# Performance work log

Measured on AMD Instinct MI355X. Metric: run time of the kernel, lower is better.

Reference implementation:

```python
import jax, jax.numpy as jnp
import numpy as np
import math

N = 20000      # nodes
E = 150000     # edges
IN = 256       # in_dim
HID = 256      # n_hid / out_dim
T = 4          # num_types
R = 8          # num_relations
H = 8          # n_heads
DK = HID // H  # d_k = 32
L = 2          # n_layers
MAXLEN = 240   # RTE max_len


def _rte_table():
    # fixed sinusoid table from RelTemporalEncoding (requires_grad=False in torch)
    pos = np.arange(MAXLEN, dtype=np.float64)[:, None]
    div = np.exp(np.arange(0, HID, 2, dtype=np.float64) * -(math.log(10000.0) / HID))
    emb = np.zeros((MAXLEN, HID), dtype=np.float64)
    emb[:, 0::2] = np.sin(pos * div) / math.sqrt(HID)
    emb[:, 1::2] = np.cos(pos * div) / math.sqrt(HID)
    return jnp.asarray(emb, dtype=jnp.float32)


def setup_inputs() -> dict:
    key = jax.random.key(0)
    ks = jax.random.split(key, 20)
    node_feature = jax.random.normal(ks[0], (N, IN), jnp.float32)
    node_type = jax.random.randint(ks[1], (N,), 0, T)
    edge_index = jax.random.randint(ks[2], (2, E), 0, N)
    edge_type = jax.random.randint(ks[3], (E,), 0, R)
    edge_time = jax.random.randint(ks[4], (E,), 0, MAXLEN)

    s_in = 1.0 / math.sqrt(IN)
    s_h = 1.0 / math.sqrt(HID)
    s_g = math.sqrt(2.0 / (DK + DK))  # glorot for relation mats

    adapt_W = jax.random.normal(ks[5], (T, IN, HID), jnp.float32) * s_in
    adapt_b = jnp.zeros((T, HID), jnp.float32)
    k_W = jax.random.normal(ks[6], (L, T, HID, HID), jnp.float32) * s_h
    k_b = jnp.zeros((L, T, HID), jnp.float32)
    q_W = jax.random.normal(ks[7], (L, T, HID, HID), jnp.float32) * s_h
    q_b = jnp.zeros((L, T, HID), jnp.float32)
    v_W = jax.random.normal(ks[8], (L, T, HID, HID), jnp.float32) * s_h
    v_b = jnp.zeros((L, T, HID), jnp.float32)
    a_W = jax.random.normal(ks[9], (L, T, HID, HID), jnp.float32) * s_h
    a_b = jnp.zeros((L, T, HID), jnp.float32)
    rel_pri = jnp.ones((L, R, H), jnp.float32)
    rel_att = jax.random.normal(ks[10], (L, R, H, DK, DK), jnp.float32) * s_g
    rel_msg = jax.random.normal(ks[11], (L, R, H, DK, DK), jnp.float32) * s_g
    skip = jnp.ones((L, T), jnp.float32)
    rte_W = jax.random.normal(ks[12], (L, HID, HID), jnp.float32) * s_h
    rte_b = jnp.zeros((L, HID), jnp.float32)
    rte_emb = _rte_table()

    return dict(node_feature=node_feature, node_type=node_type, edge_time=edge_time,
                edge_index=edge_index, edge_type=edge_type,
                adapt_W=adapt_W, adapt_b=adapt_b, k_W=k_W, k_b=k_b, q_W=q_W, q_b=q_b,
                v_W=v_W, v_b=v_b, a_W=a_W, a_b=a_b, rel_pri=rel_pri, rel_att=rel_att,
                rel_msg=rel_msg, skip=skip, rte_W=rte_W, rte_b=rte_b, rte_emb=rte_emb)


def _typed_linear(x, W, b, types):
    # x: [M, din]; W: [T, din, dout]; per-row type-selected linear (T dense GEMMs + select)
    out = jnp.zeros((x.shape[0], W.shape[-1]), x.dtype)
    for t in range(T):
        out = jnp.where((types == t)[:, None], x @ W[t] + b[t], out)
    return out


def _hgt_forward(node_feature, node_type, edge_time, edge_index, edge_type,
                 adapt_W, adapt_b, k_W, k_b, q_W, q_b, v_W, v_b, a_W, a_b,
                 rel_pri, rel_att, rel_msg, skip, rte_W, rte_b, rte_emb):
    # adapt: per-type tanh(Linear) (dropout is identity at p=0)
    x = jnp.tanh(_typed_linear(node_feature, adapt_W, adapt_b, node_type))
    src, tgt = edge_index[0], edge_index[1]   # j (source), i (target)
    st, tt = node_type[src], node_type[tgt]
    sqrt_dk = math.sqrt(DK)
    att = None
    rte = rte_emb[edge_time]                  # [E, HID]
    for l in range(L):
        x_j = x[src] + (rte @ rte_W[l] + rte_b[l])   # RTE added to source repr
        x_i = x[tgt]
        q = _typed_linear(x_i, q_W[l], q_b[l], tt).reshape(E, H, DK)
        k = _typed_linear(x_j, k_W[l], k_b[l], st).reshape(E, H, DK)
        v = _typed_linear(x_j, v_W[l], v_b[l], st).reshape(E, H, DK)
        att_e = jnp.zeros((E, H), x.dtype)
        msg = jnp.zeros((E, H, DK), x.dtype)
        for r in range(R):
            kr = jnp.einsum('ehd,hdk->ehk', k, rel_att[l, r])
            vr = jnp.einsum('ehd,hdk->ehk', v, rel_msg[l, r])
            a = (q * kr).sum(-1) * rel_pri[l, r] / sqrt_dk
            m = edge_type == r
            att_e = jnp.where(m[:, None], a, att_e)
            msg = jnp.where(m[:, None, None], vr, msg)
        # segment softmax over target node ids
        amax = jax.ops.segment_max(att_e, tgt, num_segments=N)
        ex = jnp.exp(att_e - amax[tgt])
        denom = jax.ops.segment_sum(ex, tgt, num_segments=N)
        alpha = ex / denom[tgt]                       # [E, H]
        agg = jax.ops.segment_sum(msg * alpha[:, :, None], tgt, num_segments=N)
        agg = jax.nn.gelu(agg.reshape(N, HID), approximate=False)
        trans = _typed_linear(agg, a_W[l], a_b[l], node_type)
        sk = jax.nn.sigmoid(skip[l])[node_type][:, None]
        x = trans * sk + x * (1.0 - sk)               # no LayerNorm (use_norm=False)
        att = alpha
    return att, x


def reference(node_feature, node_type, edge_time, edge_index, edge_type,
              adapt_W, adapt_b, k_W, k_b, q_W, q_b, v_W, v_b, a_W, a_b,
              rel_pri, rel_att, rel_msg, skip, rte_W, rte_b, rte_emb):
    return _hgt_forward(node_feature, node_type, edge_time, edge_index, edge_type,
                        adapt_W, adapt_b, k_W, k_b, q_W, q_b, v_W, v_b, a_W, a_b,
                        rel_pri, rel_att, rel_msg, skip, rte_W, rte_b, rte_emb)
```

## Files before the change

### kernel.cpp

```cpp
#include <hip/hip_runtime.h>
#include <hip/hip_fp16.h>

#define NN    20000
#define NE    150000
#define HD    256
#define NT    4
#define NR    8
#define NH    8
#define DKq   32
#define NL    2
#define MAXL  240
#define HBLK  256
#define SCB   ((NN + 255)/256)
#define TMAX  632
#define FOLDN 79
#define FOLDC 15
#define INV_SQRT_DK 0.17677669529663687f

typedef _Float16 f16x4 __attribute__((ext_vector_type(4)));
typedef float    f32x4v __attribute__((ext_vector_type(4)));

__global__ __launch_bounds__(256) void k_nhist(const int* __restrict__ ntype, int* __restrict__ nhist)
{
    __shared__ int h[NT];
    const int tid = threadIdx.x, b = blockIdx.x;
    if (tid < NT) h[tid] = 0;
    __syncthreads();
    const int cn = (NN + HBLK-1)/HBLK;
    const int nEnd = min((b+1)*cn, NN);
    for (int i = b*cn + tid; i < nEnd; i += 256) atomicAdd(&h[ntype[i]], 1);
    __syncthreads();
    if (tid < NT) nhist[b*NT + tid] = h[tid];
}
__global__ void k_nscan(const int* __restrict__ nhist, int* __restrict__ noff, int* __restrict__ nbase,
                        int* __restrict__ tlist, int* __restrict__ tcount)
{
    __shared__ int tot[NT];
    const int tid = threadIdx.x;
    if (tid < NT){
        int s = 0;
        for (int b = 0; b < HBLK; b++) s += nhist[b*NT + tid];
        tot[tid] = s;
    }
    __syncthreads();
    if (tid == 0){ noff[0]=0; for (int t=0;t<NT;t++) noff[t+1]=noff[t]+tot[t]; }
    if (tid < NT){
        int base = 0; for (int t=0;t<tid;t++) base += tot[t];
        int run = 0;
        for (int b=0;b<HBLK;b++){ nbase[b*NT+tid] = base + run; run += nhist[b*NT+tid]; }
    }
    __syncthreads();
    if (tid == 0){
        int c = 0;
        for (int t = 0; t < NT; t++){
            const int ntile = (tot[t] + 31) >> 5;
            for (int rt = 0; rt < ntile; rt++) tlist[c++] = (t << 20) | rt;
        }
        *tcount = c;
    }
}
__global__ __launch_bounds__(256) void k_nscatter(const int* __restrict__ ntype,
    const int* __restrict__ nbase, int* __restrict__ nbucket)
{
    __shared__ int cur[NT];
    const int tid = threadIdx.x, b = blockIdx.x;
    if (tid < NT) cur[tid] = nbase[b*NT + tid];
    __syncthreads();
    const int cn = (NN + HBLK-1)/HBLK;
    const int nEnd = min((b+1)*cn, NN);
    for (int i = b*cn + tid; i < nEnd; i += 256)
        nbucket[atomicAdd(&cur[ntype[i]], 1)] = i;
}

__global__ void k_zero_bins(int* __restrict__ cnt){
    int i = blockIdx.x*256 + threadIdx.x;
    if (i < NN) cnt[i] = 0;
}
__global__ void k_csr_hist(const int* __restrict__ ei, int* __restrict__ cnt){
    int e = blockIdx.x*256 + threadIdx.x;
    if (e >= NE) return;
    atomicAdd(&cnt[ei[NE+e]], 1);
}
__global__ __launch_bounds__(256) void k_scan1(const int* __restrict__ cnt,
    int* __restrict__ tgt_off, int* __restrict__ bsum)
{
    __shared__ int sh[256];
    const int t = threadIdx.x, b = blockIdx.x;
    const int i = b*256 + t;
    const int v = (i < NN) ? cnt[i] : 0;
    sh[t] = v;
    __syncthreads();
    #pragma unroll
    for (int d = 1; d < 256; d <<= 1){
        const int u = (t >= d) ? sh[t-d] : 0;
        __syncthreads();
        sh[t] += u;
        __syncthreads();
    }
    if (i < NN) tgt_off[i] = sh[t] - v;
    if (t == 255) bsum[b] = sh[255];
}
__global__ __launch_bounds__(128) void k_scan2(const int* __restrict__ bsum,
    int* __restrict__ bbase, int* __restrict__ tgt_off)
{
    __shared__ int sh[128];
    const int t = threadIdx.x;
    const int v = (t < SCB) ? bsum[t] : 0;
    sh[t] = v;
    __syncthreads();
    #pragma unroll
    for (int d = 1; d < 128; d <<= 1){
        const int u = (t >= d) ? sh[t-d] : 0;
        __syncthreads();
        sh[t] += u;
        __syncthreads();
    }
    if (t < SCB) bbase[t] = sh[t] - v;
    if (t == 0) tgt_off[NN] = NE;
}
__global__ __launch_bounds__(256) void k_scan3(int* __restrict__ tgt_off,
    const int* __restrict__ bbase, int* __restrict__ binCur)
{
    const int i = blockIdx.x*256 + threadIdx.x;
    if (i >= NN) return;
    const int o = tgt_off[i] + bbase[blockIdx.x];
    tgt_off[i] = o;
    binCur[i] = o;
}
__global__ void k_csr_scatter(const int* __restrict__ ei, const int* __restrict__ etype,
    const int* __restrict__ etime, const int* __restrict__ ntype,
    int* __restrict__ binCur, int* __restrict__ src_s, int* __restrict__ combo_s,
    int* __restrict__ eid_s, int* __restrict__ tgt_s)
{
    int e = blockIdx.x*256 + threadIdx.x;
    if (e >= NE) return;
    const int tgt = ei[NE+e], r = etype[e], src = ei[e];
    const int pos = atomicAdd(&binCur[tgt], 1);
    src_s[pos] = src;
    combo_s[pos] = (etime[e]*NT + ntype[src]) | (r << 12);
    eid_s[pos] = e;
    tgt_s[pos] = tgt;
}

__global__ __launch_bounds__(256) void k_w2f16_big(
    const float* __restrict__ adaptW, const float* __restrict__ qW, const float* __restrict__ kW,
    const float* __restrict__ vW, const float* __restrict__ aW, _Float16* __restrict__ out)
{
    const int y = blockIdx.y;
    const float* src; int m;
    if (y < 4){ src = adaptW; m = y; }
    else if (y < 12){ src = qW; m = y-4; }
    else if (y < 20){ src = kW; m = y-12; }
    else if (y < 28){ src = vW; m = y-20; }
    else { src = aW; m = y-28; }
    const float* ip = src + (size_t)m*65536;
    _Float16* op = out + (size_t)y*65536;
    const int tid4 = blockIdx.x*256 + threadIdx.x;
    const int k4 = tid4 >> 8, c = tid4 & 255;
    f16x4 hv;
    #pragma unroll
    for (int j = 0; j < 4; j++)
        hv[j] = (_Float16)ip[(size_t)(((k4*4 + j) << 8) + c)];
    *reinterpret_cast<f16x4*>(&op[(size_t)tid4 * 4]) = hv;
}
__global__ __launch_bounds__(256) void k_w2f16_rel(
    const float* __restrict__ attW, const float* __restrict__ msgW, _Float16* __restrict__ out)
{
    const int y = blockIdx.y;
    const float* ip = (y < 128) ? (attW + (size_t)y*1024) : (msgW + (size_t)(y-128)*1024);
    _Float16* op = out + (size_t)y*1024;
    const int tid4 = threadIdx.x;
    const int k4 = tid4 >> 5, c = tid4 & 31;
    f16x4 hv;
    #pragma unroll
    for (int j = 0; j < 4; j++)
        hv[j] = (_Float16)ip[(size_t)(((k4*4 + j) << 5) + c)];
    *reinterpret_cast<f16x4*>(&op[(size_t)tid4 * 4]) = hv;
}

__global__ __launch_bounds__(256) void k_typed_fused(
    const float* __restrict__ inF, const _Float16* __restrict__ inH,
    const _Float16* __restrict__ Wa, const float* __restrict__ ba, void* __restrict__ oa,
    const _Float16* __restrict__ Wq, const float* __restrict__ bq, void* __restrict__ oq,
    const _Float16* __restrict__ Wk, const float* __restrict__ bk, void* __restrict__ ok_,
    const _Float16* __restrict__ Wv, const float* __restrict__ bv, void* __restrict__ ov,
    const int* __restrict__ nbucket, const int* __restrict__ noff,
    const int* __restrict__ tlist, const int* __restrict__ tcount,
    int mode, int ohmask, const float* __restrict__ skipv, const float* __restrict__ xold)
{
    if ((int)blockIdx.x >= *tcount) return;
    const int ent = tlist[blockIdx.x];
    const int t = ent >> 20, rowTile = ent & 0xFFFFF;
    const int start = noff[t], cnt = noff[t+1] - start;

    const int tid = threadIdx.x;
    const int w = tid >> 6, lane = tid & 63;
    const int lrow = lane & 15, lgrp = lane >> 4;

    __shared__ _Float16 Al[32][260];
    __shared__ int nid[32];

    if (tid < 32){
        const int gr = rowTile*32 + tid;
        nid[tid] = (gr < cnt) ? nbucket[start + gr] : -1;
    }
    __syncthreads();

    {
        const int r = tid >> 3;
        const int arow = nid[r];
        if (inH){
            const _Float16* ap = (arow >= 0) ? (inH + (size_t)arow*HD) : nullptr;
            #pragma unroll
            for (int j = 0; j < 8; j++){
                const int f4 = (tid & 7) + j*8;
                f16x4 hv = {0,0,0,0};
                if (ap) hv = *reinterpret_cast<const f16x4*>(ap + f4*4);
                *reinterpret_cast<f16x4*>(&Al[r][f4*4]) = hv;
            }
        } else {
            const float* ap = (arow >= 0) ? (inF + (size_t)arow*HD) : nullptr;
            #pragma unroll
            for (int j = 0; j < 8; j++){
                const int f4 = (tid & 7) + j*8;
                float4 v = make_float4(0.f,0.f,0.f,0.f);
                if (ap) v = *reinterpret_cast<const float4*>(ap + f4*4);
                f16x4 hv;
                hv[0]=(_Float16)v.x; hv[1]=(_Float16)v.y; hv[2]=(_Float16)v.z; hv[3]=(_Float16)v.w;
                *reinterpret_cast<f16x4*>(&Al[r][f4*4]) = hv;
            }
        }
    }
    __syncthreads();

    float sk = 0.f;
    if (mode == 2) sk = 1.f/(1.f + __expf(-skipv[t]));

    const bool chain = (Wq != nullptr);

    auto proc = [&](const _Float16* Wb, const float* bb, void* out, int oh, int md, bool cw){
        const _Float16* W = Wb + (size_t)t*HD*HD;
        const float* bias = bb + (size_t)t*HD;
        f32x4v acc[4][2];
        #pragma unroll
        for (int cs = 0; cs < 4; cs++){
            acc[cs][0] = (f32x4v){0.f,0.f,0.f,0.f};
            acc[cs][1] = (f32x4v){0.f,0.f,0.f,0.f};
        }
        #pragma unroll 4
        for (int kc = 0; kc < 16; kc++){
            f16x4 bf[4];
            #pragma unroll
            for (int cs = 0; cs < 4; cs++)
                bf[cs] = *reinterpret_cast<const f16x4*>(
                    &W[(size_t)((kc*4 + lgrp)*HD + w*64 + cs*16 + lrow)*4]);
            const f16x4 af0 = *reinterpret_cast<const f16x4*>(&Al[lrow][kc*16 + lgrp*4]);
            const f16x4 af1 = *reinterpret_cast<const f16x4*>(&Al[16 + lrow][kc*16 + lgrp*4]);
            #pragma unroll
            for (int cs = 0; cs < 4; cs++){
                acc[cs][0] = __builtin_amdgcn_mfma_f32_16x16x16f16(af0, bf[cs], acc[cs][0], 0,0,0);
                acc[cs][1] = __builtin_amdgcn_mfma_f32_16x16x16f16(af1, bf[cs], acc[cs][1], 0,0,0);
            }
        }
        if (cw) __syncthreads();
        #pragma unroll
        for (int cs = 0; cs < 4; cs++){
            const int col = w*64 + cs*16 + lrow;
            const float bcol = bias[col];
            #pragma unroll
            for (int rt = 0; rt < 2; rt++){
                #pragma unroll
                for (int i = 0; i < 4; i++){
                    const int lr = rt*16 + lgrp*4 + i;
                    const int gr = rowTile*32 + lr;
                    if (gr >= cnt) continue;
                    const int node = nid[lr];
                    float v = acc[cs][rt][i] + bcol;
                    if (md == 1) v = tanhf(v);
                    else if (md == 2){
                        const float xo = xold[(size_t)node*HD + col];
                        v = v*sk + xo*(1.f - sk);
                    }
                    if (oh) ((_Float16*)out)[(size_t)node*HD + col] = (_Float16)v;
                    else    ((float*)out)[(size_t)node*HD + col] = v;
                    if (cw) Al[lr][col] = (_Float16)v;
                }
            }
        }
        if (cw) __syncthreads();
    };

    proc(Wa, ba, oa, ohmask & 1, mode, chain);
    if (chain){
        proc(Wq, bq, oq, (ohmask >> 1) & 1, 0, false);
        proc(Wk, bk, ok_, (ohmask >> 2) & 1, 0, false);
        proc(Wv, bv, ov, (ohmask >> 3) & 1, 0, false);
    }
}

__global__ __launch_bounds__(256) void k_row_gemm(
    const float* __restrict__ A, const float* __restrict__ W, const float* __restrict__ bias,
    float* __restrict__ C)
{
    const int row = blockIdx.x, d = threadIdx.x;
    __shared__ float ar[HD];
    ar[d] = A[(size_t)row*HD + d];
    __syncthreads();
    float acc = bias[d];
    #pragma unroll 8
    for (int k=0;k<HD;k++) acc = fmaf(ar[k], W[(size_t)k*HD + d], acc);
    C[(size_t)row*HD + d] = acc;
}
__global__ __launch_bounds__(256) void k_row_gemm2(
    const float* __restrict__ A, const float* __restrict__ kWb, const float* __restrict__ vWb,
    _Float16* __restrict__ Kc, _Float16* __restrict__ Vc)
{
    const int row = blockIdx.x, ty = blockIdx.y, d = threadIdx.x;
    const float* W = ((blockIdx.z == 0) ? kWb : vWb) + (size_t)ty*HD*HD;
    _Float16* C = (blockIdx.z == 0) ? Kc : Vc;
    __shared__ float ar[HD];
    ar[d] = A[(size_t)row*HD + d];
    __syncthreads();
    float acc = 0.f;
    #pragma unroll 8
    for (int k=0;k<HD;k++) acc = fmaf(ar[k], W[(size_t)k*HD + d], acc);
    C[(size_t)row*(NT*HD) + ty*HD + d] = (_Float16)acc;
}

__global__ __launch_bounds__(256) void k_fold_mfma(
    const _Float16* __restrict__ IN, const _Float16* __restrict__ MATF,
    _Float16* __restrict__ OUT, int M, int nbx)
{
    const int r = blockIdx.y;
    const int lane = threadIdx.x & 63, w = threadIdx.x >> 6;
    const int lrow = lane & 15, lgrp = lane >> 4;
    f16x4 b[NH][2][2];
    const _Float16* Mr = MATF + (size_t)r*NH*1024;
    #pragma unroll
    for (int h = 0; h < NH; h++)
      #pragma unroll
      for (int kb = 0; kb < 2; kb++)
        #pragma unroll
        for (int hf = 0; hf < 2; hf++)
            b[h][kb][hf] = *reinterpret_cast<const f16x4*>(
                &Mr[(size_t)h*1024 + (size_t)(((kb*4 + lgrp)*32) + hf*16 + lrow)*4]);
    const int ntiles = M >> 4;
    for (int t = (int)blockIdx.x*4 + w; t < ntiles; t += nbx*4){
        const int row0 = t*16;
        const _Float16* inrow = IN + (size_t)(row0 + lrow)*HD;
        f16x4 a[NH][2];
        #pragma unroll
        for (int h = 0; h < NH; h++)
          #pragma unroll
          for (int kb = 0; kb < 2; kb++)
              a[h][kb] = *reinterpret_cast<const f16x4*>(&inrow[h*32 + kb*16 + lgrp*4]);
        #pragma unroll
        for (int h = 0; h < NH; h++){
          #pragma unroll
          for (int hf = 0; hf < 2; hf++){
              f32x4v acc = {0.f,0.f,0.f,0.f};
              acc = __builtin_amdgcn_mfma_f32_16x16x16f16(a[h][0], b[h][0][hf], acc, 0,0,0);
              acc = __builtin_amdgcn_mfma_f32_16x16x16f16(a[h][1], b[h][1][hf], acc, 0,0,0);
              #pragma unroll
              for (int i = 0; i < 4; i++){
                  const int rr = lgrp*4 + i;
                  OUT[((size_t)(row0+rr)*NR + r)*HD + h*32 + hf*16 + lrow] = (_Float16)acc[i];
              }
          }
        }
    }
}

__global__ __launch_bounds__(256) void k_score(
    const float* __restrict__ q0, const _Float16* __restrict__ kA, const _Float16* __restrict__ KcA,
    const float* __restrict__ relP,
    const int* __restrict__ src_s, const int* __restrict__ combo_s, const int* __restrict__ tgt_s,
    float* __restrict__ s_arr)
{
    const int j = blockIdx.x*4 + (threadIdx.x >> 6);
    if (j >= NE) return;
    const int lane = threadIdx.x & 63;
    const int h = lane >> 3, c4 = (lane & 7) << 2;
    const int src = src_s[j];
    const int cw  = combo_s[j];
    const int tgt = tgt_s[j];
    const int r = cw >> 12, combo = cw & 0xFFF;

    const float4 q4 = *reinterpret_cast<const float4*>(&q0[(size_t)tgt*HD + h*32 + c4]);
    const f16x4 ka = *reinterpret_cast<const f16x4*>(&kA[((size_t)src*NR + r)*HD + h*32 + c4]);
    const f16x4 kc = *reinterpret_cast<const f16x4*>(&KcA[((size_t)combo*NR + r)*HD + h*32 + c4]);
    float v = q4.x*((float)ka[0]+(float)kc[0])
            + q4.y*((float)ka[1]+(float)kc[1])
            + q4.z*((float)ka[2]+(float)kc[2])
            + q4.w*((float)ka[3]+(float)kc[3]);
    v += __shfl_xor(v, 1); v += __shfl_xor(v, 2); v += __shfl_xor(v, 4);
    if ((lane & 7) == 0)
        s_arr[(size_t)j*NH + h] = v * relP[r*NH + h] * INV_SQRT_DK;
}

__global__ __launch_bounds__(256) void k_softmax(
    float* __restrict__ s_arr, const int* __restrict__ tgt_off, const int* __restrict__ eid_s,
    float* __restrict__ out_att, int store)
{
    const int idx = blockIdx.x*256 + threadIdx.x;
    if (idx >= NN*NH) return;
    const int n = idx >> 3, h = idx & 7;
    const int e0 = tgt_off[n], e1 = tgt_off[n+1];
    if (e0 == e1) return;
    float m = -INFINITY;
    for (int j = e0; j < e1; j++) m = fmaxf(m, s_arr[(size_t)j*NH + h]);
    float l = 0.f;
    for (int j = e0; j < e1; j++) l += __expf(s_arr[(size_t)j*NH + h] - m);
    const float inv = 1.f / l;
    for (int j = e0; j < e1; j++){
        const float a = __expf(s_arr[(size_t)j*NH + h] - m) * inv;
        s_arr[(size_t)j*NH + h] = a;
        if (store) out_att[(size_t)eid_s[j]*NH + h] = a;
    }
}

__global__ __launch_bounds__(256) void k_agg(
    const _Float16* __restrict__ vM, const _Float16* __restrict__ VcM,
    const float* __restrict__ alpha,
    const int* __restrict__ tgt_off, const int* __restrict__ src_s, const int* __restrict__ combo_s,
    _Float16* __restrict__ agg)
{
    const int n = blockIdx.x*4 + (threadIdx.x >> 6);
    if (n >= NN) return;
    const int lane = threadIdx.x & 63;
    const int h = lane >> 3, c4 = (lane & 7) << 2;
    const int col = h*32 + c4;
    const int e0 = tgt_off[n], e1 = tgt_off[n+1];
    float a0=0.f, a1=0.f, a2=0.f, a3=0.f;
    for (int j = e0; j < e1; j++){
        const int src = src_s[j];
        const int cw  = combo_s[j];
        const int r = cw >> 12, combo = cw & 0xFFF;
        const float al = alpha[(size_t)j*NH + h];
        const f16x4 vm = *reinterpret_cast<const f16x4*>(&vM[((size_t)src*NR + r)*HD + col]);
        const f16x4 vc = *reinterpret_cast<const f16x4*>(&VcM[((size_t)combo*NR + r)*HD + col]);
        a0 = fmaf(al, (float)vm[0] + (float)vc[0], a0);
        a1 = fmaf(al, (float)vm[1] + (float)vc[1], a1);
        a2 = fmaf(al, (float)vm[2] + (float)vc[2], a2);
        a3 = fmaf(al, (float)vm[3] + (float)vc[3], a3);
    }
    f16x4 o;
    o[0] = (_Float16)(0.5f*a0*(1.f + erff(a0*0.70710678118654752f)));
    o[1] = (_Float16)(0.5f*a1*(1.f + erff(a1*0.70710678118654752f)));
    o[2] = (_Float16)(0.5f*a2*(1.f + erff(a2*0.70710678118654752f)));
    o[3] = (_Float16)(0.5f*a3*(1.f + erff(a3*0.70710678118654752f)));
    *reinterpret_cast<f16x4*>(&agg[(size_t)n*HD + col]) = o;
}

extern "C" void kernel_launch(void* const* d_in, const int* in_sizes, int n_in,
                              void* d_out, int out_size, void* d_ws, size_t ws_size,
                              hipStream_t stream)
{
    const float* node_feature = (const float*)d_in[0];
    const int*   node_type    = (const int*)d_in[1];
    const int*   edge_time    = (const int*)d_in[2];
    const int*   edge_index   = (const int*)d_in[3];
    const int*   edge_type    = (const int*)d_in[4];
    const float* adapt_W = (const float*)d_in[5];
    const float* adapt_b = (const float*)d_in[6];
    const float* k_W = (const float*)d_in[7];
    const float* k_b = (const float*)d_in[8];
    const float* q_W = (const float*)d_in[9];
    const float* q_b = (const float*)d_in[10];
    const float* v_W = (const float*)d_in[11];
    const float* v_b = (const float*)d_in[12];
    const float* a_W = (const float*)d_in[13];
    const float* a_b = (const float*)d_in[14];
    const float* rel_pri = (const float*)d_in[15];
    const float* rel_att = (const float*)d_in[16];
    const float* rel_msg = (const float*)d_in[17];
    const float* skip  = (const float*)d_in[18];
    const float* rte_W = (const float*)d_in[19];
    const float* rte_b = (const float*)d_in[20];
    const float* rte_emb = (const float*)d_in[21];

    char* wp = (char*)d_ws;
    auto alloc_f = [&](size_t n)->float*{ float* p=(float*)wp; wp += n*sizeof(float); return p; };
    auto alloc_i = [&](size_t n)->int*  { int*   p=(int*)wp;   wp += n*sizeof(int);   return p; };
    auto alloc_h = [&](size_t n)->_Float16*{ _Float16* p=(_Float16*)wp; wp += n*sizeof(_Float16); return p; };
    float* xA    = alloc_f((size_t)NN*HD);
    float* xB    = alloc_f((size_t)NN*HD);
    float* q0f   = alloc_f((size_t)NN*HD);
    _Float16* k0h = alloc_h((size_t)NN*HD);
    _Float16* v0h = alloc_h((size_t)NN*HD);
    _Float16* aggh= alloc_h((size_t)NN*HD);
    float* s_arr = alloc_f((size_t)NE*NH);
    float* rteP  = alloc_f((size_t)MAXL*HD);
    _Float16* Kch = alloc_h((size_t)MAXL*NT*HD);
    _Float16* Vch = alloc_h((size_t)MAXL*NT*HD);
    _Float16* kavm = alloc_h((size_t)NN*NR*HD);
    _Float16* kcaA0 = alloc_h((size_t)MAXL*NT*NR*HD);
    _Float16* kcaA1 = alloc_h((size_t)MAXL*NT*NR*HD);
    _Float16* kcaM0 = alloc_h((size_t)MAXL*NT*NR*HD);
    _Float16* kcaM1 = alloc_h((size_t)MAXL*NT*NR*HD);
    _Float16* wF   = alloc_h((size_t)36*65536);
    _Float16* relF = alloc_h((size_t)256*1024);
    int* nbucket = alloc_i(NN);
    int* nhist   = alloc_i(HBLK*NT);
    int* nbase   = alloc_i(HBLK*NT);
    int* noff    = alloc_i(8);
    int* tlist   = alloc_i(TMAX);
    int* tcount  = alloc_i(8);
    int* cnt     = alloc_i(NN);
    int* bsum    = alloc_i(SCB);
    int* bbase   = alloc_i(SCB);
    int* binCur  = alloc_i(NN);
    int* tgt_off = alloc_i(NN+1);
    int* src_s   = alloc_i(NE);
    int* combo_s = alloc_i(NE);
    int* eid_s   = alloc_i(NE);
    int* tgt_s   = alloc_i(NE);

    const _Float16* adaptF = wF;
    const _Float16* qF = wF + (size_t)4*65536;
    const _Float16* kF = wF + (size_t)12*65536;
    const _Float16* vF = wF + (size_t)20*65536;
    const _Float16* aF = wF + (size_t)28*65536;
    const _Float16* relAF = relF;
    const _Float16* relMF = relF + (size_t)128*1024;

    float* out_att = (float*)d_out;
    float* out_x   = (float*)d_out + (size_t)NE*NH;

    const dim3 gFoldN(FOLDN, NR);
    const dim3 gFoldC(FOLDC, NR);
    const int gE256 = (NE + 255)/256;
    const int gSc = (NE + 3)/4;
    const int gSm = (NN*NH + 255)/256;
    const int gAg = (NN + 3)/4;

    k_w2f16_big<<<dim3(64,36),256,0,stream>>>(adapt_W, q_W, k_W, v_W, a_W, wF);
    k_w2f16_rel<<<dim3(1,256),256,0,stream>>>(rel_att, rel_msg, relF);

    k_nhist<<<HBLK,256,0,stream>>>(node_type, nhist);
    k_nscan<<<1,64,0,stream>>>(nhist, noff, nbase, tlist, tcount);
    k_nscatter<<<HBLK,256,0,stream>>>(node_type, nbase, nbucket);

    k_zero_bins<<<SCB,256,0,stream>>>(cnt);
    k_csr_hist<<<gE256,256,0,stream>>>(edge_index, cnt);
    k_scan1<<<SCB,256,0,stream>>>(cnt, tgt_off, bsum);
    k_scan2<<<1,128,0,stream>>>(bsum, bbase, tgt_off);
    k_scan3<<<SCB,256,0,stream>>>(tgt_off, bbase, binCur);
    k_csr_scatter<<<gE256,256,0,stream>>>(edge_index, edge_type, edge_time, node_type,
                                          binCur, src_s, combo_s, eid_s, tgt_s);

    {
        k_row_gemm<<<MAXL,256,0,stream>>>(rte_emb, rte_W, rte_b, rteP);
        k_row_gemm2<<<dim3(MAXL,NT,2),256,0,stream>>>(rteP, k_W, v_W, Kch, Vch);
        k_fold_mfma<<<gFoldC,256,0,stream>>>(Kch, relAF, kcaA0, MAXL*NT, FOLDC);
        k_fold_mfma<<<gFoldC,256,0,stream>>>(Vch, relMF, kcaM0, MAXL*NT, FOLDC);
        k_row_gemm<<<MAXL,256,0,stream>>>(rte_emb, rte_W + (size_t)HD*HD, rte_b + HD, rteP);
        k_row_gemm2<<<dim3(MAXL,NT,2),256,0,stream>>>(rteP, k_W + (size_t)NT*HD*HD,
                                                      v_W + (size_t)NT*HD*HD, Kch, Vch);
        k_fold_mfma<<<gFoldC,256,0,stream>>>(Kch, relAF + (size_t)NR*NH*1024, kcaA1, MAXL*NT, FOLDC);
        k_fold_mfma<<<gFoldC,256,0,stream>>>(Vch, relMF + (size_t)NR*NH*1024, kcaM1, MAXL*NT, FOLDC);
    }

    k_typed_fused<<<TMAX,256,0,stream>>>(node_feature, nullptr,
                                         adaptF, adapt_b, xA,
                                         qF, q_b, q0f,
                                         kF, k_b, k0h,
                                         vF, v_b, v0h,
                                         nbucket, noff, tlist, tcount,
                                         1, 12, nullptr, nullptr);

    for (int l = 0; l < NL; l++){
        const _Float16* rAF = relAF + (size_t)l*NR*NH*1024;
        const _Float16* rMF = relMF + (size_t)l*NR*NH*1024;
        const _Float16* kcaA = (l == 0) ? kcaA0 : kcaA1;
        const _Float16* kcaM = (l == 0) ? kcaM0 : kcaM1;
        k_fold_mfma<<<gFoldN,256,0,stream>>>(k0h, rAF, kavm, NN, FOLDN);
        k_score<<<gSc,256,0,stream>>>(q0f, kavm, kcaA, rel_pri + (size_t)l*NR*NH,
                                      src_s, combo_s, tgt_s, s_arr);
        const int store_s = (l == NL-1) ? 1 : 0;
        k_softmax<<<gSm,256,0,stream>>>(s_arr, tgt_off, eid_s, out_att, store_s);
        k_fold_mfma<<<gFoldN,256,0,stream>>>(v0h, rMF, kavm, NN, FOLDN);
        k_agg<<<gAg,256,0,stream>>>(kavm, kcaM, s_arr, tgt_off, src_s, combo_s, aggh);
        if (l == 0){
            k_typed_fused<<<TMAX,256,0,stream>>>(nullptr, aggh,
                                                 aF, a_b, xB,
                                                 qF + (size_t)NT*HD*HD, q_b + (size_t)NT*HD, q0f,
                                                 kF + (size_t)NT*HD*HD, k_b + (size_t)NT*HD, k0h,
                                                 vF + (size_t)NT*HD*HD, v_b + (size_t)NT*HD, v0h,
                                                 nbucket, noff, tlist, tcount,
                                                 2, 12, skip, xA);
        } else {
            k_typed_fused<<<TMAX,256,0,stream>>>(nullptr, aggh,
                                                 aF + (size_t)NT*HD*HD, a_b + (size_t)NT*HD, out_x,
                                                 nullptr, nullptr, nullptr,
                                                 nullptr, nullptr, nullptr,
                                                 nullptr, nullptr, nullptr,
                                                 nbucket, noff, tlist, tcount,
                                                 2, 0, skip + NT, xB);
        }
    }
}
```

Baseline: 597.3 us.

## Fuse edge scoring and segment softmax into one per-target-node kernel

Replaces the per-edge score kernel and the separate per-(node,head) softmax kernel with a single kernel where one wavefront handles one target node. It computes scores over that node's CSR edge range, tracks the running max, then has one lane per head do the exp, sum and normalise passes. The query row is loaded once per node instead of once per edge, and the tgt_s array and its scatter write are removed. The cost is serial work per node and load imbalance on high-degree nodes, and the softmax passes use only 8 of 64 lanes.

```diff
diff --git a/kernel.cpp b/kernel.cpp
--- a/kernel.cpp
+++ b/kernel.cpp
@@ -130,7 +130,7 @@
 __global__ void k_csr_scatter(const int* __restrict__ ei, const int* __restrict__ etype,
     const int* __restrict__ etime, const int* __restrict__ ntype,
     int* __restrict__ binCur, int* __restrict__ src_s, int* __restrict__ combo_s,
-    int* __restrict__ eid_s, int* __restrict__ tgt_s)
+    int* __restrict__ eid_s)
 {
     int e = blockIdx.x*256 + threadIdx.x;
     if (e >= NE) return;
@@ -139,7 +139,6 @@
     src_s[pos] = src;
     combo_s[pos] = (etime[e]*NT + ntype[src]) | (r << 12);
     eid_s[pos] = e;
-    tgt_s[pos] = tgt;
 }
 
 __global__ __launch_bounds__(256) void k_w2f16_big(
@@ -371,51 +370,51 @@
     }
 }
 
-__global__ __launch_bounds__(256) void k_score(
+__global__ __launch_bounds__(256) void k_scoresm(
     const float* __restrict__ q0, const _Float16* __restrict__ kA, const _Float16* __restrict__ KcA,
     const float* __restrict__ relP,
-    const int* __restrict__ src_s, const int* __restrict__ combo_s, const int* __restrict__ tgt_s,
-    float* __restrict__ s_arr)
-{
-    const int j = blockIdx.x*4 + (threadIdx.x >> 6);
-    if (j >= NE) return;
+    const int* __restrict__ tgt_off, const int* __restrict__ src_s, const int* __restrict__ combo_s,
+    const int* __restrict__ eid_s,
+    float* __restrict__ s_arr, float* __restrict__ out_att, int store_s)
+{
+    const int n = blockIdx.x*4 + (threadIdx.x >> 6);
+    if (n >= NN) return;
     const int lane = threadIdx.x & 63;
     const int h = lane >> 3, c4 = (lane & 7) << 2;
-    const int src = src_s[j];
-    const int cw  = combo_s[j];
-    const int tgt = tgt_s[j];
-    const int r = cw >> 12, combo = cw & 0xFFF;
-
-    const float4 q4 = *reinterpret_cast<const float4*>(&q0[(size_t)tgt*HD + h*32 + c4]);
-    const f16x4 ka = *reinterpret_cast<const f16x4*>(&kA[((size_t)src*NR + r)*HD + h*32 + c4]);
-    const f16x4 kc = *reinterpret_cast<const f16x4*>(&KcA[((size_t)combo*NR + r)*HD + h*32 + c4]);
-    float v = q4.x*((float)ka[0]+(float)kc[0])
-            + q4.y*((float)ka[1]+(float)kc[1])
-            + q4.z*((float)ka[2]+(float)kc[2])
-            + q4.w*((float)ka[3]+(float)kc[3]);
-    v += __shfl_xor(v, 1); v += __shfl_xor(v, 2); v += __shfl_xor(v, 4);
-    if ((lane & 7) == 0)
-        s_arr[(size_t)j*NH + h] = v * relP[r*NH + h] * INV_SQRT_DK;
-}
-
-__global__ __launch_bounds__(256) void k_softmax(
-    float* __restrict__ s_arr, const int* __restrict__ tgt_off, const int* __restrict__ eid_s,
-    float* __restrict__ out_att, int store)
-{
-    const int idx = blockIdx.x*256 + threadIdx.x;
-    if (idx >= NN*NH) return;
-    const int n = idx >> 3, h = idx & 7;
+    const int col = h*32 + c4;
     const int e0 = tgt_off[n], e1 = tgt_off[n+1];
     if (e0 == e1) return;
+
+    const float4 q4 = *reinterpret_cast<const float4*>(&q0[(size_t)n*HD + col]);
     float m = -INFINITY;
-    for (int j = e0; j < e1; j++) m = fmaxf(m, s_arr[(size_t)j*NH + h]);
-    float l = 0.f;
-    for (int j = e0; j < e1; j++) l += __expf(s_arr[(size_t)j*NH + h] - m);
-    const float inv = 1.f / l;
     for (int j = e0; j < e1; j++){
-        const float a = __expf(s_arr[(size_t)j*NH + h] - m) * inv;
-        s_arr[(size_t)j*NH + h] = a;
-        if (store) out_att[(size_t)eid_s[j]*NH + h] = a;
+        const int src = src_s[j];
+        const int cw  = combo_s[j];
+        const int r = cw >> 12, combo = cw & 0xFFF;
+        const f16x4 ka = *reinterpret_cast<const f16x4*>(&kA[((size_t)src*NR + r)*HD + col]);
+        const f16x4 kc = *reinterpret_cast<const f16x4*>(&KcA[((size_t)combo*NR + r)*HD + col]);
+        float s = q4.x*((float)ka[0]+(float)kc[0])
+                + q4.y*((float)ka[1]+(float)kc[1])
+                + q4.z*((float)ka[2]+(float)kc[2])
+                + q4.w*((float)ka[3]+(float)kc[3]);
+        s += __shfl_xor(s, 1); s += __shfl_xor(s, 2); s += __shfl_xor(s, 4);
+        s *= relP[r*NH + h] * INV_SQRT_DK;
+        if ((lane & 7) == 0) s_arr[(size_t)j*NH + h] = s;
+        m = fmaxf(m, s);
+    }
+    if ((lane & 7) == 0){
+        float l = 0.f;
+        for (int j = e0; j < e1; j++){
+            const float e = __expf(s_arr[(size_t)j*NH + h] - m);
+            s_arr[(size_t)j*NH + h] = e;
+            l += e;
+        }
+        const float inv = 1.f / l;
+        for (int j = e0; j < e1; j++){
+            const float a = s_arr[(size_t)j*NH + h] * inv;
+            s_arr[(size_t)j*NH + h] = a;
+            if (store_s) out_att[(size_t)eid_s[j]*NH + h] = a;
+        }
     }
 }
 
@@ -514,7 +513,6 @@
     int* src_s   = alloc_i(NE);
     int* combo_s = alloc_i(NE);
     int* eid_s   = alloc_i(NE);
-    int* tgt_s   = alloc_i(NE);
 
     const _Float16* adaptF = wF;
     const _Float16* qF = wF + (size_t)4*65536;
@@ -530,9 +528,7 @@
     const dim3 gFoldN(FOLDN, NR);
     const dim3 gFoldC(FOLDC, NR);
     const int gE256 = (NE + 255)/256;
-    const int gSc = (NE + 3)/4;
-    const int gSm = (NN*NH + 255)/256;
-    const int gAg = (NN + 3)/4;
+    const int gEg = (NN + 3)/4;
 
     k_w2f16_big<<<dim3(64,36),256,0,stream>>>(adapt_W, q_W, k_W, v_W, a_W, wF);
     k_w2f16_rel<<<dim3(1,256),256,0,stream>>>(rel_att, rel_msg, relF);
@@ -547,7 +543,7 @@
     k_scan2<<<1,128,0,stream>>>(bsum, bbase, tgt_off);
     k_scan3<<<SCB,256,0,stream>>>(tgt_off, bbase, binCur);
     k_csr_scatter<<<gE256,256,0,stream>>>(edge_index, edge_type, edge_time, node_type,
-                                          binCur, src_s, combo_s, eid_s, tgt_s);
+                                          binCur, src_s, combo_s, eid_s);
 
     {
         k_row_gemm<<<MAXL,256,0,stream>>>(rte_emb, rte_W, rte_b, rteP);
@@ -574,13 +570,13 @@
         const _Float16* rMF = relMF + (size_t)l*NR*NH*1024;
         const _Float16* kcaA = (l == 0) ? kcaA0 : kcaA1;
         const _Float16* kcaM = (l == 0) ? kcaM0 : kcaM1;
+        const int store_s = (l == NL-1) ? 1 : 0;
         k_fold_mfma<<<gFoldN,256,0,stream>>>(k0h, rAF, kavm, NN, FOLDN);
-        k_score<<<gSc,256,0,stream>>>(q0f, kavm, kcaA, rel_pri + (size_t)l*NR*NH,
-                                      src_s, combo_s, tgt_s, s_arr);
-        const int store_s = (l == NL-1) ? 1 : 0;
-        k_softmax<<<gSm,256,0,stream>>>(s_arr, tgt_off, eid_s, out_att, store_s);
+        k_scoresm<<<gEg,256,0,stream>>>(q0f, kavm, kcaA, rel_pri + (size_t)l*NR*NH,
+                                        tgt_off, src_s, combo_s, eid_s,
+                                        s_arr, out_att, store_s);
         k_fold_mfma<<<gFoldN,256,0,stream>>>(v0h, rMF, kavm, NN, FOLDN);
-        k_agg<<<gAg,256,0,stream>>>(kavm, kcaM, s_arr, tgt_off, src_s, combo_s, aggh);
+        k_agg<<<gEg,256,0,stream>>>(kavm, kcaM, s_arr, tgt_off, src_s, combo_s, aggh);
         if (l == 0){
             k_typed_fused<<<TMAX,256,0,stream>>>(nullptr, aggh,
                                                  aF, a_b, xB,
```

Measured after the change: 599.8 us. About the same (+0.4%).
